# Performance work log

Measured on AMD Instinct MI355X. Metric: run time of the kernel, lower is better.

## Reference

```python
import jax, jax.numpy as jnp
import numpy as np

B, N, D = 8, 2048, 768


def setup_inputs() -> dict:
    key = jax.random.key(0)
    ks = jax.random.split(key, 12)
    s = 1.0 / np.sqrt(D)
    inp = {
        "query": jax.random.normal(ks[0], (B, N, D), dtype=jnp.float32),
        "value": jax.random.normal(ks[1], (B, N, D), dtype=jnp.float32),
        "mask": jax.random.randint(ks[2], (B, N), 0, 2, dtype=jnp.int32),
        "q_w": jax.random.uniform(ks[3], (D, D), jnp.float32, -s, s),
        "q_b": jax.random.uniform(ks[4], (D,), jnp.float32, -s, s),
        "k_w": jax.random.uniform(ks[5], (D, D), jnp.float32, -s, s),
        "k_b": jax.random.uniform(ks[6], (D,), jnp.float32, -s, s),
        "v_w": jax.random.uniform(ks[7], (D, D), jnp.float32, -s, s),
        "v_b": jax.random.uniform(ks[8], (D,), jnp.float32, -s, s),
        "fc_w": jax.random.uniform(ks[9], (D, D), jnp.float32, -s, s),
        "fc_b": jax.random.uniform(ks[10], (D,), jnp.float32, -s, s),
    }
    # guarantee at least one unmasked key per batch to avoid all--inf softmax rows
    inp["mask"] = inp["mask"].at[:, 0].set(1)
    return inp


def reference(query, value, mask, q_w, q_b, k_w, k_b, v_w, v_b, fc_w, fc_b):
    # torch Linear: y = x @ W.T + b  (dim==768 branch of the module)
    q = jnp.einsum("bnd,ed->bne", query, q_w) + q_b   # [B,N,D]
    k = jnp.einsum("bnd,ed->bne", value, k_w) + k_b   # [B,N,D]
    v = jnp.einsum("bnd,ed->bne", value, v_w) + v_b   # [B,N,D]
    # unscaled scores, as in the original (no 1/sqrt(d))
    scores = jnp.einsum("bqd,bkd->bqk", q, k)         # [B,N,N]
    key_mask = mask[:, None, :] != 0                  # [B,1,N]
    scores = jnp.where(key_mask, scores, -jnp.inf)
    attn = jax.nn.softmax(scores, axis=2)
    merged = jnp.einsum("bqk,bkd->bqd", attn, v)      # [B,N,D]
    merged = merged * mask[:, :, None].astype(merged.dtype)
    return jnp.einsum("bnd,ed->bne", merged, fc_w) + fc_b
```

## Files before the change

### kernel.cpp

```cpp
#include <hip/hip_runtime.h>
#include <hip/hip_bf16.h>

using bf16 = __hip_bfloat16;
typedef __attribute__((ext_vector_type(4))) float f32x4;
typedef __attribute__((ext_vector_type(8))) __bf16 bf16x8;
typedef __attribute__((ext_vector_type(4))) unsigned int u32x4;
typedef unsigned short u16;

#define LOG2E 1.4426950408889634f
#define SHIFT2 69.24936192747498f

__device__ __forceinline__ void gload_lds16(const void* g, void* l) {
  __builtin_amdgcn_global_load_lds((const __attribute__((address_space(1))) void*)g,
                                   (__attribute__((address_space(3))) void*)l, 16, 0, 0);
}

__device__ __forceinline__ bf16x8 lds_frag(const bf16* p) {
  u32x4 u = *(const u32x4*)p;
  return __builtin_bit_cast(bf16x8, u);
}

__device__ __forceinline__ u16 bf_bits(float v) {
  return __builtin_bit_cast(u16, __float2bfloat16(v));
}

template<int AMODE, bool SPLIT, int CMODE, bool BIAS, bool RSCALE,
         bool MGATHER, bool CSCAT, bool RAGK, bool NCHECK>
__global__ __launch_bounds__(256, 2) void gemm_nt(
    const void* __restrict__ Ah_, const void* __restrict__ Al_, long lda, long strideA,
    const bf16* __restrict__ Bh_, const bf16* __restrict__ Bl_, long ldb, long strideB,
    void* __restrict__ Ch_, void* __restrict__ Cl_, long ldc, long strideC,
    int Kparam,
    const float* __restrict__ bias,
    float* __restrict__ rowsum, long rsStride,
    const int* __restrict__ idxp, const int* __restrict__ cntp)
{
  const int tid = threadIdx.x;
  const int lane15 = tid & 15;
  const int quad = (tid >> 4) & 3;
  const int wave = tid >> 6;
  const int wm = (wave >> 1) * 64;
  const int wn = (wave & 1) * 64;
  const long z = blockIdx.z;
  const long m0 = (long)blockIdx.y * 128;
  const long n0 = (long)blockIdx.x * 128;

  int cnt = 1 << 30;
  if (cntp) {
    cnt = cntp[z];
    if (m0 >= cnt) return;
    if constexpr (NCHECK) { if (n0 >= cnt) return; }
  }
  const int K = RAGK ? ((cnt + 127) & ~127) : Kparam;

  constexpr int KW = SPLIT ? 64 : 32;
  __shared__ alignas(16) bf16 As[128 * KW];
  __shared__ alignas(16) bf16 Bs[128 * KW];
  __shared__ float rowacc[128];

  const bf16* Bbh = Bh_ + z * strideB;
  const bf16* Bbl = SPLIT ? (Bl_ + z * strideB) : nullptr;

  const bf16* Abh = nullptr; const bf16* Abl = nullptr;
  const float* Af = nullptr;
  if constexpr (AMODE == 0) {
    Abh = (const bf16*)Ah_ + z * strideA;
    if constexpr (SPLIT) Abl = (const bf16*)Al_ + z * strideA;
  } else {
    Af = (const float*)Ah_ + z * strideA;
  }

  const int arow = tid >> 1;
  const int ahalf = tid & 1;
  const int aflip = arow & 1;
  const int aswz = (arow >> 1) & 3;
  long agrow = m0 + arow;
  if constexpr (AMODE == 1 && MGATHER) agrow = idxp[z * 2048 + m0 + arow];

  f32x4 acc[4][4];
  #pragma unroll
  for (int i = 0; i < 4; ++i)
    #pragma unroll
    for (int j = 0; j < 4; ++j) acc[i][j] = (f32x4){0.f, 0.f, 0.f, 0.f};

  for (int k0 = 0; k0 < K; k0 += 32) {
    __syncthreads();
    if constexpr (SPLIT) {
      #pragma unroll
      for (int r = 0; r < 4; ++r) {
        const int idx = r * 256 + tid, row = idx >> 3, slot = idx & 7;
        const int flip = row & 1, sw = (row >> 1) & 3;
        const int h = (slot >> 2) ^ flip, s = (slot & 3) ^ sw;
        const bf16* g = (h ? Bbl : Bbh) + (n0 + row) * ldb + k0 + s * 8;
        gload_lds16(g, &Bs[idx * 8]);
      }
    } else {
      #pragma unroll
      for (int r = 0; r < 2; ++r) {
        const int idx = r * 256 + tid, row = idx >> 2, slot = idx & 3;
        const int sw = (row >> 1) & 3;
        gload_lds16(Bbh + (n0 + row) * ldb + k0 + (slot ^ sw) * 8, &Bs[idx * 8]);
      }
    }
    if constexpr (AMODE == 0) {
      if constexpr (SPLIT) {
        #pragma unroll
        for (int r = 0; r < 4; ++r) {
          const int idx = r * 256 + tid, row = idx >> 3, slot = idx & 7;
          const int flip = row & 1, sw = (row >> 1) & 3;
          const int h = (slot >> 2) ^ flip, s = (slot & 3) ^ sw;
          const bf16* g = (h ? Abl : Abh) + (m0 + row) * lda + k0 + s * 8;
          gload_lds16(g, &As[idx * 8]);
        }
      } else {
        #pragma unroll
        for (int r = 0; r < 2; ++r) {
          const int idx = r * 256 + tid, row = idx >> 2, slot = idx & 3;
          const int sw = (row >> 1) & 3;
          gload_lds16(Abh + (m0 + row) * lda + k0 + (slot ^ sw) * 8, &As[idx * 8]);
        }
      }
    } else {
      const float* src = Af + agrow * lda + k0;
      #pragma unroll
      for (int ss = 0; ss < 2; ++ss) {
        const int s = ahalf * 2 + ss;
        float tv[8];
        *(f32x4*)tv       = *(const f32x4*)(src + s * 8);
        *(f32x4*)(tv + 4) = *(const f32x4*)(src + s * 8 + 4);
        u32x4 hi, lo;
        u16* ph = (u16*)&hi; u16* pl = (u16*)&lo;
        #pragma unroll
        for (int j = 0; j < 8; ++j) {
          bf16 hb = __float2bfloat16(tv[j]);
          ph[j] = __builtin_bit_cast(u16, hb);
          if constexpr (SPLIT) pl[j] = bf_bits(tv[j] - __bfloat162float(hb));
        }
        if constexpr (SPLIT) {
          const int sh = (aflip << 2) | (s ^ aswz);
          *(u32x4*)&As[arow * 64 + sh * 8] = hi;
          *(u32x4*)&As[arow * 64 + (sh ^ 4) * 8] = lo;
        } else {
          *(u32x4*)&As[arow * 32 + (s ^ aswz) * 8] = hi;
        }
      }
    }
    __syncthreads();

    const int swl = (lane15 >> 1) & 3;
    if constexpr (SPLIT) {
      const int eff = ((lane15 & 1) << 2) | (quad ^ swl);
      bf16x8 ah[4], al[4], bh[4], bl[4];
      #pragma unroll
      for (int t = 0; t < 4; ++t) {
        const int ar = (wm + t * 16 + lane15) * 64;
        const int br = (wn + t * 16 + lane15) * 64;
        ah[t] = lds_frag(&As[ar + eff * 8]);
        al[t] = lds_frag(&As[ar + (eff ^ 4) * 8]);
        bh[t] = lds_frag(&Bs[br + eff * 8]);
        bl[t] = lds_frag(&Bs[br + (eff ^ 4) * 8]);
      }
      #pragma unroll
      for (int i = 0; i < 4; ++i)
        #pragma unroll
        for (int j = 0; j < 4; ++j) {
          acc[i][j] = __builtin_amdgcn_mfma_f32_16x16x32_bf16(ah[i], bh[j], acc[i][j], 0, 0, 0);
          acc[i][j] = __builtin_amdgcn_mfma_f32_16x16x32_bf16(al[i], bh[j], acc[i][j], 0, 0, 0);
          acc[i][j] = __builtin_amdgcn_mfma_f32_16x16x32_bf16(ah[i], bl[j], acc[i][j], 0, 0, 0);
        }
    } else {
      const int eff = quad ^ swl;
      bf16x8 ah[4], bh[4];
      #pragma unroll
      for (int t = 0; t < 4; ++t) ah[t] = lds_frag(&As[(wm + t * 16 + lane15) * 32 + eff * 8]);
      #pragma unroll
      for (int t = 0; t < 4; ++t) bh[t] = lds_frag(&Bs[(wn + t * 16 + lane15) * 32 + eff * 8]);
      #pragma unroll
      for (int i = 0; i < 4; ++i)
        #pragma unroll
        for (int j = 0; j < 4; ++j)
          acc[i][j] = __builtin_amdgcn_mfma_f32_16x16x32_bf16(ah[i], bh[j], acc[i][j], 0, 0, 0);
    }
  }

  const long crow0 = m0 + wm + quad * 4;
  const long ccol0 = n0 + wn + lane15;

  if constexpr (CMODE == 3) {
    bf16* P = (bf16*)Ch_ + z * strideC;
    if (tid < 128) rowacc[tid] = 0.f;
    __syncthreads();
    bool keep[4];
    #pragma unroll
    for (int tn = 0; tn < 4; ++tn) keep[tn] = (ccol0 + tn * 16) < cnt;
    #pragma unroll
    for (int tm = 0; tm < 4; ++tm) {
      #pragma unroll
      for (int r = 0; r < 4; ++r) {
        const long row = crow0 + tm * 16 + r;
        float rsum = 0.f;
        #pragma unroll
        for (int tn = 0; tn < 4; ++tn) {
          float p = keep[tn] ? exp2f(fmaf(acc[tm][tn][r], LOG2E, -SHIFT2)) : 0.f;
          bf16 pb = __float2bfloat16(p);
          P[row * ldc + ccol0 + tn * 16] = pb;
          rsum += __bfloat162float(pb);
        }
        atomicAdd(&rowacc[(int)(row - m0)], rsum);
      }
    }
    __syncthreads();
    if (tid < 128) atomicAdd(&rowsum[z * rsStride + m0 + tid], rowacc[tid]);
    return;
  }

  float bv[4] = {0.f, 0.f, 0.f, 0.f};
  if constexpr (BIAS) {
    #pragma unroll
    for (int tn = 0; tn < 4; ++tn) bv[tn] = bias[ccol0 + tn * 16];
  }
  if constexpr (CMODE == 2) {
    float* C = (float*)Ch_ + z * strideC;
    #pragma unroll
    for (int tm = 0; tm < 4; ++tm) {
      #pragma unroll
      for (int r = 0; r < 4; ++r) {
        const long row = crow0 + tm * 16 + r;
        long orow = row;
        bool doStore = true;
        if constexpr (CSCAT) {
          doStore = row < cnt;
          orow = doStore ? (long)idxp[z * 2048 + row] : 0;
        }
        if (doStore) {
          #pragma unroll
          for (int tn = 0; tn < 4; ++tn)
            C[orow * ldc + ccol0 + tn * 16] = acc[tm][tn][r] + bv[tn];
        }
      }
    }
  } else if constexpr (CMODE == 1) {
    bf16* Ch = (bf16*)Ch_ + z * strideC;
    bf16* Cl = (bf16*)Cl_ + z * strideC;
    #pragma unroll
    for (int tm = 0; tm < 4; ++tm) {
      const long row = crow0 + tm * 16;
      #pragma unroll
      for (int tn = 0; tn < 4; ++tn) {
        const long col = ccol0 + tn * 16;
        #pragma unroll
        for (int r = 0; r < 4; ++r) {
          float val = acc[tm][tn][r] + bv[tn];
          bf16 h = __float2bfloat16(val);
          Ch[(row + r) * ldc + col] = h;
          Cl[(row + r) * ldc + col] = __float2bfloat16(val - __bfloat162float(h));
        }
      }
    }
  } else {
    bf16* Ch = (bf16*)Ch_ + z * strideC;
    #pragma unroll
    for (int tm = 0; tm < 4; ++tm) {
      const long row = crow0 + tm * 16;
      float rm[4];
      #pragma unroll
      for (int r = 0; r < 4; ++r) {
        float f = 1.f;
        if constexpr (RSCALE) f = 1.0f / rowsum[z * rsStride + row + r];
        rm[r] = f;
      }
      #pragma unroll
      for (int tn = 0; tn < 4; ++tn) {
        const long col = ccol0 + tn * 16;
        #pragma unroll
        for (int r = 0; r < 4; ++r)
          Ch[(row + r) * ldc + col] = __float2bfloat16((acc[tm][tn][r] + bv[tn]) * rm[r]);
      }
    }
  }
}

__global__ __launch_bounds__(256) void compact_kernel(
    const int* __restrict__ mask, int* __restrict__ idx, int* __restrict__ cnt)
{
  const int z = blockIdx.x, tid = threadIdx.x;
  const int* m = mask + (long)z * 2048;
  int* id = idx + (long)z * 2048;
  int v[8]; int c = 0;
  #pragma unroll
  for (int j = 0; j < 8; ++j) { v[j] = m[tid * 8 + j]; c += (v[j] != 0) ? 1 : 0; }
  __shared__ int sc[256];
  sc[tid] = c;
  __syncthreads();
  for (int off = 1; off < 256; off <<= 1) {
    int y = 0;
    if (tid >= off) y = sc[tid - off];
    __syncthreads();
    if (tid >= off) sc[tid] += y;
    __syncthreads();
  }
  int k = sc[tid] - c;
  #pragma unroll
  for (int j = 0; j < 8; ++j)
    if (v[j]) id[k++] = tid * 8 + j;
  __syncthreads();
  const int tot = sc[255];
  if (tid == 0) cnt[z] = tot;
  const int last = id[tot - 1];
  for (int i = tot + tid; i < 2048; i += 256) id[i] = last;
}

__global__ __launch_bounds__(256) void cvt4_kernel(
    const float* __restrict__ qw, const float* __restrict__ kw,
    const float* __restrict__ vw, const float* __restrict__ fw,
    bf16* __restrict__ Wqh, bf16* __restrict__ Wql,
    bf16* __restrict__ Wkh, bf16* __restrict__ Wkl,
    bf16* __restrict__ Wvh, bf16* __restrict__ Wfh, int n8)
{
  const int i = blockIdx.x * 256 + threadIdx.x;
  if (i >= n8) return;
  const float* in; bf16* oh; bf16* ol = nullptr;
  switch (blockIdx.y) {
    case 0:  in = qw; oh = Wqh; ol = Wql; break;
    case 1:  in = kw; oh = Wkh; ol = Wkl; break;
    case 2:  in = vw; oh = Wvh; break;
    default: in = fw; oh = Wfh; break;
  }
  float tv[8];
  *(f32x4*)tv       = ((const f32x4*)in)[2 * i];
  *(f32x4*)(tv + 4) = ((const f32x4*)in)[2 * i + 1];
  u32x4 H, L;
  u16* ph = (u16*)&H; u16* pl = (u16*)&L;
  #pragma unroll
  for (int j = 0; j < 8; ++j) {
    bf16 hb = __float2bfloat16(tv[j]);
    ph[j] = __builtin_bit_cast(u16, hb);
    pl[j] = bf_bits(tv[j] - __bfloat162float(hb));
  }
  ((u32x4*)oh)[i] = H;
  if (ol) ((u32x4*)ol)[i] = L;
}

__global__ __launch_bounds__(256) void bias_fill_kernel(
    float* __restrict__ out, const float* __restrict__ fc_b)
{
  const long i = (long)blockIdx.x * 256 + threadIdx.x;
  const int col4 = (int)(i % 192);
  ((f32x4*)out)[i] = *(const f32x4*)(fc_b + col4 * 4);
}

__global__ __launch_bounds__(256) void transpose_kernel(
    const u16* __restrict__ in, u16* __restrict__ out, const int* __restrict__ cnt)
{
  const long z = blockIdx.z;
  const long r0 = (long)blockIdx.x * 64, c0 = (long)blockIdx.y * 64;
  const int kb = (cnt[z] + 127) & ~127;
  if (r0 >= kb) return;
  __shared__ alignas(16) u16 t[64][72];
  const u16* inz = in + z * 2048 * 768;
  u16* outz = out + z * 768 * 2048;
  const int tid = threadIdx.x;
  const int rr = tid >> 3, cs = (tid & 7) * 8;
  #pragma unroll
  for (int i = 0; i < 2; ++i) {
    const int row = rr + i * 32;
    u32x4 v = *(const u32x4*)(inz + (r0 + row) * 768 + c0 + cs);
    *(u32x4*)&t[row][cs] = v;
  }
  __syncthreads();
  #pragma unroll
  for (int i = 0; i < 2; ++i) {
    const int oc = rr + i * 32;
    u32x4 o;
    u16* po = (u16*)&o;
    #pragma unroll
    for (int j = 0; j < 8; ++j) po[j] = t[cs + j][oc];
    *(u32x4*)(outz + (c0 + oc) * 2048 + r0 + cs) = o;
  }
}

extern "C" void kernel_launch(void* const* d_in, const int* in_sizes, int n_in,
                              void* d_out, int out_size, void* d_ws, size_t ws_size,
                              hipStream_t stream) {
  const float* query = (const float*)d_in[0];
  const float* value = (const float*)d_in[1];
  const int*   mask  = (const int*)d_in[2];
  const float* q_w   = (const float*)d_in[3];
  const float* q_b   = (const float*)d_in[4];
  const float* k_w   = (const float*)d_in[5];
  const float* k_b   = (const float*)d_in[6];
  const float* v_w   = (const float*)d_in[7];
  const float* v_b   = (const float*)d_in[8];
  const float* fc_w  = (const float*)d_in[9];
  const float* fc_b  = (const float*)d_in[10];

  const long N = 2048, D = 768;
  const long BD = N * D;
  const int WN = (int)(D * D), W8 = WN / 8;

  char* wp = (char*)d_ws;
  auto take = [&](size_t bytes) {
    char* p = wp;
    wp += (bytes + 255) & ~(size_t)255;
    return p;
  };
  bf16* Wqh = (bf16*)take((size_t)WN * 2);
  bf16* Wql = (bf16*)take((size_t)WN * 2);
  bf16* Wkh = (bf16*)take((size_t)WN * 2);
  bf16* Wkl = (bf16*)take((size_t)WN * 2);
  bf16* Wvh = (bf16*)take((size_t)WN * 2);
  bf16* Wfh = (bf16*)take((size_t)WN * 2);
  bf16* Qh = (bf16*)take((size_t)8 * BD * 2);
  bf16* Ql = (bf16*)take((size_t)8 * BD * 2);
  bf16* Kh = (bf16*)take((size_t)8 * BD * 2);
  bf16* Kl = (bf16*)take((size_t)8 * BD * 2);
  bf16* VT = (bf16*)take((size_t)8 * BD * 2);
  bf16* P  = (bf16*)take((size_t)8 * N * N * 2);
  float* rowsum = (float*)take((size_t)8 * N * sizeof(float));
  int* idx = (int*)take((size_t)8 * N * sizeof(int));
  int* cnt = (int*)take(64);
  bf16* V = (bf16*)((char*)P + (size_t)8 * N * N * 2 - (size_t)8 * BD * 2);
  bf16* merged = Qh;

  dim3 blk(256);

  compact_kernel<<<dim3(8), blk, 0, stream>>>(mask, idx, cnt);
  cvt4_kernel<<<dim3(288, 4), blk, 0, stream>>>(q_w, k_w, v_w, fc_w,
      Wqh, Wql, Wkh, Wkl, Wvh, Wfh, W8);
  hipMemsetAsync(rowsum, 0, (size_t)8 * N * sizeof(float), stream);
  bias_fill_kernel<<<dim3(12288), blk, 0, stream>>>((float*)d_out, fc_b);

  gemm_nt<1, true, 1, true, false, true, false, false, false><<<dim3(6, 16, 8), blk, 0, stream>>>(
      query, nullptr, D, BD, Wqh, Wql, D, 0, Qh, Ql, D, BD, (int)D,
      q_b, nullptr, 0, idx, cnt);
  gemm_nt<1, true, 1, true, false, true, false, false, false><<<dim3(6, 16, 8), blk, 0, stream>>>(
      value, nullptr, D, BD, Wkh, Wkl, D, 0, Kh, Kl, D, BD, (int)D,
      k_b, nullptr, 0, idx, cnt);
  gemm_nt<1, false, 0, true, false, true, false, false, false><<<dim3(6, 16, 8), blk, 0, stream>>>(
      value, nullptr, D, BD, Wvh, nullptr, D, 0, V, nullptr, D, BD, (int)D,
      v_b, nullptr, 0, idx, cnt);
  transpose_kernel<<<dim3(32, 12, 8), blk, 0, stream>>>((const u16*)V, (u16*)VT, cnt);

  gemm_nt<0, true, 3, false, false, false, false, false, true><<<dim3(16, 16, 8), blk, 0, stream>>>(
      Qh, Ql, D, BD, Kh, Kl, D, BD, P, nullptr, N, N * N, (int)D,
      nullptr, rowsum, N, nullptr, cnt);
  gemm_nt<0, false, 0, false, true, false, false, true, false><<<dim3(6, 16, 8), blk, 0, stream>>>(
      P, nullptr, N, N * N, VT, nullptr, N, BD, merged, nullptr, D, BD, 0,
      nullptr, rowsum, N, nullptr, cnt);
  gemm_nt<0, false, 2, true, false, false, true, false, false><<<dim3(6, 16, 8), blk, 0, stream>>>(
      merged, nullptr, D, BD, Wfh, nullptr, D, 0, d_out, nullptr, D, BD, (int)D,
      fc_b, nullptr, 0, idx, cnt);
}
```

Measured before the change: 456.1 us.

## Use persistent compacted tile scheduling for GEMMs and fuse Q/K projections

Converts the batched GEMM kernel into a persistent-grid kernel that enumerates only the valid tiles per batch, derived from the masked-row counts, and loops over them with a fixed 512-block grid. Early-exit blocks for padded rows and columns are no longer launched. The Q and K projection GEMMs are merged into one launch through secondary pointers. The per-tile linear search over batch prefix sums and the extra syncs add some overhead, and fixed grid sizing may leave load imbalance.

```diff
diff --git a/kernel.cpp b/kernel.cpp
--- a/kernel.cpp
+++ b/kernel.cpp
@@ -24,16 +24,21 @@
   return __builtin_bit_cast(u16, __float2bfloat16(v));
 }
 
+struct GArgs {
+  const void* Ah; const void* Al; long lda; long strideA;
+  const bf16* Bh; const bf16* Bl; long ldb; long strideB;
+  void* Ch; void* Cl; long ldc; long strideC;
+  int K;
+  const float* bias;
+  float* rowsum; long rsStride;
+  const int* idx; const int* cnt;
+  const void* Ah2; const bf16* Bh2; const bf16* Bl2;
+  void* Ch2; void* Cl2; const float* bias2;
+};
+
 template<int AMODE, bool SPLIT, int CMODE, bool BIAS, bool RSCALE,
-         bool MGATHER, bool CSCAT, bool RAGK, bool NCHECK>
-__global__ __launch_bounds__(256, 2) void gemm_nt(
-    const void* __restrict__ Ah_, const void* __restrict__ Al_, long lda, long strideA,
-    const bf16* __restrict__ Bh_, const bf16* __restrict__ Bl_, long ldb, long strideB,
-    void* __restrict__ Ch_, void* __restrict__ Cl_, long ldc, long strideC,
-    int Kparam,
-    const float* __restrict__ bias,
-    float* __restrict__ rowsum, long rsStride,
-    const int* __restrict__ idxp, const int* __restrict__ cntp)
+         bool MGATHER, bool CSCAT, bool SQUARE, bool RAGK, bool QK2>
+__global__ __launch_bounds__(256, 2) void gemm_nt(GArgs ga)
 {
   const int tid = threadIdx.x;
   const int lane15 = tid & 15;
@@ -41,240 +46,265 @@
   const int wave = tid >> 6;
   const int wm = (wave >> 1) * 64;
   const int wn = (wave & 1) * 64;
-  const long z = blockIdx.z;
-  const long m0 = (long)blockIdx.y * 128;
-  const long n0 = (long)blockIdx.x * 128;
-
-  int cnt = 1 << 30;
-  if (cntp) {
-    cnt = cntp[z];
-    if (m0 >= cnt) return;
-    if constexpr (NCHECK) { if (n0 >= cnt) return; }
-  }
-  const int K = RAGK ? ((cnt + 127) & ~127) : Kparam;
-
+
+  constexpr int NZ = QK2 ? 16 : 8;
   constexpr int KW = SPLIT ? 64 : 32;
   __shared__ alignas(16) bf16 As[128 * KW];
   __shared__ alignas(16) bf16 Bs[128 * KW];
   __shared__ float rowacc[128];
-
-  const bf16* Bbh = Bh_ + z * strideB;
-  const bf16* Bbl = SPLIT ? (Bl_ + z * strideB) : nullptr;
-
-  const bf16* Abh = nullptr; const bf16* Abl = nullptr;
-  const float* Af = nullptr;
-  if constexpr (AMODE == 0) {
-    Abh = (const bf16*)Ah_ + z * strideA;
-    if constexpr (SPLIT) Abl = (const bf16*)Al_ + z * strideA;
-  } else {
-    Af = (const float*)Ah_ + z * strideA;
-  }
+  __shared__ int sT[8];
+  __shared__ int sTz[NZ];
+
+  if (tid < 8) sT[tid] = (ga.cnt[tid] + 127) >> 7;
+  __syncthreads();
+  if (tid < NZ) {
+    const int Tm = sT[QK2 ? (tid & 7) : tid];
+    sTz[tid] = SQUARE ? Tm * Tm : Tm * 6;
+  }
+  __syncthreads();
+  int total = 0;
+  #pragma unroll
+  for (int i = 0; i < NZ; ++i) total += sTz[i];
 
   const int arow = tid >> 1;
   const int ahalf = tid & 1;
   const int aflip = arow & 1;
   const int aswz = (arow >> 1) & 3;
-  long agrow = m0 + arow;
-  if constexpr (AMODE == 1 && MGATHER) agrow = idxp[z * 2048 + m0 + arow];
-
-  f32x4 acc[4][4];
-  #pragma unroll
-  for (int i = 0; i < 4; ++i)
+
+  for (int t = blockIdx.x; t < total; t += gridDim.x) {
+    int vz = 0, rem = t;
+    while (rem >= sTz[vz]) { rem -= sTz[vz]; ++vz; }
+    const int z = QK2 ? (vz & 7) : vz;
+    const int mat = QK2 ? (vz >> 3) : 0;
+    const int Tm = sT[z];
+    int mt, nt;
+    if constexpr (SQUARE) { mt = rem / Tm; nt = rem - mt * Tm; }
+    else                  { mt = rem / 6;  nt = rem - mt * 6; }
+    const long m0 = (long)mt * 128;
+    const long n0 = (long)nt * 128;
+    const int cnt = ga.cnt[z];
+    const int K = RAGK ? Tm * 128 : ga.K;
+
+    const bf16* Bh = (QK2 && mat) ? ga.Bh2 : ga.Bh;
+    const bf16* Bl = (QK2 && mat) ? ga.Bl2 : ga.Bl;
+    const bf16* Bbh = Bh + z * ga.strideB;
+    const bf16* Bbl = SPLIT ? (Bl + z * ga.strideB) : nullptr;
+
+    const bf16* Abh = nullptr; const bf16* Abl = nullptr;
+    const float* Af = nullptr;
+    {
+      const void* Ahp = (QK2 && mat) ? ga.Ah2 : ga.Ah;
+      if constexpr (AMODE == 0) {
+        Abh = (const bf16*)Ahp + (long)z * ga.strideA;
+        if constexpr (SPLIT) Abl = (const bf16*)ga.Al + (long)z * ga.strideA;
+      } else {
+        Af = (const float*)Ahp + (long)z * ga.strideA;
+      }
+    }
+    long agrow = m0 + arow;
+    if constexpr (AMODE == 1 && MGATHER) agrow = ga.idx[(long)z * 2048 + m0 + arow];
+
+    f32x4 acc[4][4];
     #pragma unroll
-    for (int j = 0; j < 4; ++j) acc[i][j] = (f32x4){0.f, 0.f, 0.f, 0.f};
-
-  for (int k0 = 0; k0 < K; k0 += 32) {
-    __syncthreads();
-    if constexpr (SPLIT) {
-      #pragma unroll
-      for (int r = 0; r < 4; ++r) {
-        const int idx = r * 256 + tid, row = idx >> 3, slot = idx & 7;
-        const int flip = row & 1, sw = (row >> 1) & 3;
-        const int h = (slot >> 2) ^ flip, s = (slot & 3) ^ sw;
-        const bf16* g = (h ? Bbl : Bbh) + (n0 + row) * ldb + k0 + s * 8;
-        gload_lds16(g, &Bs[idx * 8]);
-      }
-    } else {
-      #pragma unroll
-      for (int r = 0; r < 2; ++r) {
-        const int idx = r * 256 + tid, row = idx >> 2, slot = idx & 3;
-        const int sw = (row >> 1) & 3;
-        gload_lds16(Bbh + (n0 + row) * ldb + k0 + (slot ^ sw) * 8, &Bs[idx * 8]);
-      }
-    }
-    if constexpr (AMODE == 0) {
+    for (int i = 0; i < 4; ++i)
+      #pragma unroll
+      for (int j = 0; j < 4; ++j) acc[i][j] = (f32x4){0.f, 0.f, 0.f, 0.f};
+
+    for (int k0 = 0; k0 < K; k0 += 32) {
+      __syncthreads();
       if constexpr (SPLIT) {
         #pragma unroll
         for (int r = 0; r < 4; ++r) {
           const int idx = r * 256 + tid, row = idx >> 3, slot = idx & 7;
           const int flip = row & 1, sw = (row >> 1) & 3;
           const int h = (slot >> 2) ^ flip, s = (slot & 3) ^ sw;
-          const bf16* g = (h ? Abl : Abh) + (m0 + row) * lda + k0 + s * 8;
-          gload_lds16(g, &As[idx * 8]);
+          const bf16* g = (h ? Bbl : Bbh) + (n0 + row) * ga.ldb + k0 + s * 8;
+          gload_lds16(g, &Bs[idx * 8]);
         }
       } else {
         #pragma unroll
         for (int r = 0; r < 2; ++r) {
           const int idx = r * 256 + tid, row = idx >> 2, slot = idx & 3;
           const int sw = (row >> 1) & 3;
-          gload_lds16(Abh + (m0 + row) * lda + k0 + (slot ^ sw) * 8, &As[idx * 8]);
+          gload_lds16(Bbh + (n0 + row) * ga.ldb + k0 + (slot ^ sw) * 8, &Bs[idx * 8]);
+        }
+      }
+      if constexpr (AMODE == 0) {
+        if constexpr (SPLIT) {
+          #pragma unroll
+          for (int r = 0; r < 4; ++r) {
+            const int idx = r * 256 + tid, row = idx >> 3, slot = idx & 7;
+            const int flip = row & 1, sw = (row >> 1) & 3;
+            const int h = (slot >> 2) ^ flip, s = (slot & 3) ^ sw;
+            const bf16* g = (h ? Abl : Abh) + (m0 + row) * ga.lda + k0 + s * 8;
+            gload_lds16(g, &As[idx * 8]);
+          }
+        } else {
+          #pragma unroll
+          for (int r = 0; r < 2; ++r) {
+            const int idx = r * 256 + tid, row = idx >> 2, slot = idx & 3;
+            const int sw = (row >> 1) & 3;
+            gload_lds16(Abh + (m0 + row) * ga.lda + k0 + (slot ^ sw) * 8, &As[idx * 8]);
+          }
+        }
+      } else {
+        const float* src = Af + agrow * ga.lda + k0;
+        #pragma unroll
+        for (int ss = 0; ss < 2; ++ss) {
+          const int s = ahalf * 2 + ss;
+          float tv[8];
+          *(f32x4*)tv       = *(const f32x4*)(src + s * 8);
+          *(f32x4*)(tv + 4) = *(const f32x4*)(src + s * 8 + 4);
+          u32x4 hi, lo;
+          u16* ph = (u16*)&hi; u16* pl = (u16*)&lo;
+          #pragma unroll
+          for (int j = 0; j < 8; ++j) {
+            bf16 hb = __float2bfloat16(tv[j]);
+            ph[j] = __builtin_bit_cast(u16, hb);
+            if constexpr (SPLIT) pl[j] = bf_bits(tv[j] - __bfloat162float(hb));
+          }
+          if constexpr (SPLIT) {
+            const int sh = (aflip << 2) | (s ^ aswz);
+            *(u32x4*)&As[arow * 64 + sh * 8] = hi;
+            *(u32x4*)&As[arow * 64 + (sh ^ 4) * 8] = lo;
+          } else {
+            *(u32x4*)&As[arow * 32 + (s ^ aswz) * 8] = hi;
+          }
+        }
+      }
+      __syncthreads();
+
+      const int swl = (lane15 >> 1) & 3;
+      if constexpr (SPLIT) {
+        const int eff = ((lane15 & 1) << 2) | (quad ^ swl);
+        bf16x8 ah[4], al[4], bh[4], bl[4];
+        #pragma unroll
+        for (int tt = 0; tt < 4; ++tt) {
+          const int ar = (wm + tt * 16 + lane15) * 64;
+          const int br = (wn + tt * 16 + lane15) * 64;
+          ah[tt] = lds_frag(&As[ar + eff * 8]);
+          al[tt] = lds_frag(&As[ar + (eff ^ 4) * 8]);
+          bh[tt] = lds_frag(&Bs[br + eff * 8]);
+          bl[tt] = lds_frag(&Bs[br + (eff ^ 4) * 8]);
+        }
+        #pragma unroll
+        for (int i = 0; i < 4; ++i)
+          #pragma unroll
+          for (int j = 0; j < 4; ++j) {
+            acc[i][j] = __builtin_amdgcn_mfma_f32_16x16x32_bf16(ah[i], bh[j], acc[i][j], 0, 0, 0);
+            acc[i][j] = __builtin_amdgcn_mfma_f32_16x16x32_bf16(al[i], bh[j], acc[i][j], 0, 0, 0);
+            acc[i][j] = __builtin_amdgcn_mfma_f32_16x16x32_bf16(ah[i], bl[j], acc[i][j], 0, 0, 0);
+          }
+      } else {
+        const int eff = quad ^ swl;
+        bf16x8 ah[4], bh[4];
+        #pragma unroll
+        for (int tt = 0; tt < 4; ++tt) ah[tt] = lds_frag(&As[(wm + tt * 16 + lane15) * 32 + eff * 8]);
+        #pragma unroll
+        for (int tt = 0; tt < 4; ++tt) bh[tt] = lds_frag(&Bs[(wn + tt * 16 + lane15) * 32 + eff * 8]);
+        #pragma unroll
+        for (int i = 0; i < 4; ++i)
+          #pragma unroll
+          for (int j = 0; j < 4; ++j)
+            acc[i][j] = __builtin_amdgcn_mfma_f32_16x16x32_bf16(ah[i], bh[j], acc[i][j], 0, 0, 0);
+      }
+    }
+
+    const long crow0 = m0 + wm + quad * 4;
+    const long ccol0 = n0 + wn + lane15;
+
+    if constexpr (CMODE == 3) {
+      bf16* P = (bf16*)ga.Ch + (long)z * ga.strideC;
+      __syncthreads();
+      if (tid < 128) rowacc[tid] = 0.f;
+      __syncthreads();
+      bool keep[4];
+      #pragma unroll
+      for (int tn = 0; tn < 4; ++tn) keep[tn] = (ccol0 + tn * 16) < cnt;
+      #pragma unroll
+      for (int tm = 0; tm < 4; ++tm) {
+        #pragma unroll
+        for (int r = 0; r < 4; ++r) {
+          const long row = crow0 + tm * 16 + r;
+          float rsum = 0.f;
+          #pragma unroll
+          for (int tn = 0; tn < 4; ++tn) {
+            float p = keep[tn] ? exp2f(fmaf(acc[tm][tn][r], LOG2E, -SHIFT2)) : 0.f;
+            bf16 pb = __float2bfloat16(p);
+            P[row * ga.ldc + ccol0 + tn * 16] = pb;
+            rsum += __bfloat162float(pb);
+          }
+          atomicAdd(&rowacc[(int)(row - m0)], rsum);
+        }
+      }
+      __syncthreads();
+      if (tid < 128) atomicAdd(&ga.rowsum[z * ga.rsStride + m0 + tid], rowacc[tid]);
+      continue;
+    }
+
+    const float* bias = (QK2 && mat) ? ga.bias2 : ga.bias;
+    float bv[4] = {0.f, 0.f, 0.f, 0.f};
+    if constexpr (BIAS) {
+      #pragma unroll
+      for (int tn = 0; tn < 4; ++tn) bv[tn] = bias[ccol0 + tn * 16];
+    }
+    if constexpr (CMODE == 2) {
+      float* C = (float*)ga.Ch + (long)z * ga.strideC;
+      #pragma unroll
+      for (int tm = 0; tm < 4; ++tm) {
+        #pragma unroll
+        for (int r = 0; r < 4; ++r) {
+          const long row = crow0 + tm * 16 + r;
+          long orow = row;
+          bool doStore = true;
+          if constexpr (CSCAT) {
+            doStore = row < cnt;
+            orow = doStore ? (long)ga.idx[(long)z * 2048 + row] : 0;
+          }
+          if (doStore) {
+            #pragma unroll
+            for (int tn = 0; tn < 4; ++tn)
+              C[orow * ga.ldc + ccol0 + tn * 16] = acc[tm][tn][r] + bv[tn];
+          }
+        }
+      }
+    } else if constexpr (CMODE == 1) {
+      bf16* Ch = (bf16*)((QK2 && mat) ? ga.Ch2 : ga.Ch) + (long)z * ga.strideC;
+      bf16* Cl = (bf16*)((QK2 && mat) ? ga.Cl2 : ga.Cl) + (long)z * ga.strideC;
+      #pragma unroll
+      for (int tm = 0; tm < 4; ++tm) {
+        const long row = crow0 + tm * 16;
+        #pragma unroll
+        for (int tn = 0; tn < 4; ++tn) {
+          const long col = ccol0 + tn * 16;
+          #pragma unroll
+          for (int r = 0; r < 4; ++r) {
+            float val = acc[tm][tn][r] + bv[tn];
+            bf16 h = __float2bfloat16(val);
+            Ch[(row + r) * ga.ldc + col] = h;
+            Cl[(row + r) * ga.ldc + col] = __float2bfloat16(val - __bfloat162float(h));
+          }
         }
       }
     } else {
-      const float* src = Af + agrow * lda + k0;
-      #pragma unroll
-      for (int ss = 0; ss < 2; ++ss) {
-        const int s = ahalf * 2 + ss;
-        float tv[8];
-        *(f32x4*)tv       = *(const f32x4*)(src + s * 8);
-        *(f32x4*)(tv + 4) = *(const f32x4*)(src + s * 8 + 4);
-        u32x4 hi, lo;
-        u16* ph = (u16*)&hi; u16* pl = (u16*)&lo;
-        #pragma unroll
-        for (int j = 0; j < 8; ++j) {
-          bf16 hb = __float2bfloat16(tv[j]);
-          ph[j] = __builtin_bit_cast(u16, hb);
-          if constexpr (SPLIT) pl[j] = bf_bits(tv[j] - __bfloat162float(hb));
-        }
-        if constexpr (SPLIT) {
-          const int sh = (aflip << 2) | (s ^ aswz);
-          *(u32x4*)&As[arow * 64 + sh * 8] = hi;
-          *(u32x4*)&As[arow * 64 + (sh ^ 4) * 8] = lo;
-        } else {
-          *(u32x4*)&As[arow * 32 + (s ^ aswz) * 8] = hi;
-        }
-      }
-    }
-    __syncthreads();
-
-    const int swl = (lane15 >> 1) & 3;
-    if constexpr (SPLIT) {
-      const int eff = ((lane15 & 1) << 2) | (quad ^ swl);
-      bf16x8 ah[4], al[4], bh[4], bl[4];
-      #pragma unroll
-      for (int t = 0; t < 4; ++t) {
-        const int ar = (wm + t * 16 + lane15) * 64;
-        const int br = (wn + t * 16 + lane15) * 64;
-        ah[t] = lds_frag(&As[ar + eff * 8]);
-        al[t] = lds_frag(&As[ar + (eff ^ 4) * 8]);
-        bh[t] = lds_frag(&Bs[br + eff * 8]);
-        bl[t] = lds_frag(&Bs[br + (eff ^ 4) * 8]);
-      }
-      #pragma unroll
-      for (int i = 0; i < 4; ++i)
-        #pragma unroll
-        for (int j = 0; j < 4; ++j) {
-          acc[i][j] = __builtin_amdgcn_mfma_f32_16x16x32_bf16(ah[i], bh[j], acc[i][j], 0, 0, 0);
-          acc[i][j] = __builtin_amdgcn_mfma_f32_16x16x32_bf16(al[i], bh[j], acc[i][j], 0, 0, 0);
-          acc[i][j] = __builtin_amdgcn_mfma_f32_16x16x32_bf16(ah[i], bl[j], acc[i][j], 0, 0, 0);
-        }
-    } else {
-      const int eff = quad ^ swl;
-      bf16x8 ah[4], bh[4];
-      #pragma unroll
-      for (int t = 0; t < 4; ++t) ah[t] = lds_frag(&As[(wm + t * 16 + lane15) * 32 + eff * 8]);
-      #pragma unroll
-      for (int t = 0; t < 4; ++t) bh[t] = lds_frag(&Bs[(wn + t * 16 + lane15) * 32 + eff * 8]);
-      #pragma unroll
-      for (int i = 0; i < 4; ++i)
-        #pragma unroll
-        for (int j = 0; j < 4; ++j)
-          acc[i][j] = __builtin_amdgcn_mfma_f32_16x16x32_bf16(ah[i], bh[j], acc[i][j], 0, 0, 0);
-    }
-  }
-
-  const long crow0 = m0 + wm + quad * 4;
-  const long ccol0 = n0 + wn + lane15;
-
-  if constexpr (CMODE == 3) {
-    bf16* P = (bf16*)Ch_ + z * strideC;
-    if (tid < 128) rowacc[tid] = 0.f;
-    __syncthreads();
-    bool keep[4];
-    #pragma unroll
-    for (int tn = 0; tn < 4; ++tn) keep[tn] = (ccol0 + tn * 16) < cnt;
-    #pragma unroll
-    for (int tm = 0; tm < 4; ++tm) {
-      #pragma unroll
-      for (int r = 0; r < 4; ++r) {
-        const long row = crow0 + tm * 16 + r;
-        float rsum = 0.f;
+      bf16* Ch = (bf16*)ga.Ch + (long)z * ga.strideC;
+      #pragma unroll
+      for (int tm = 0; tm < 4; ++tm) {
+        const long row = crow0 + tm * 16;
+        float rm[4];
+        #pragma unroll
+        for (int r = 0; r < 4; ++r) {
+          float f = 1.f;
+          if constexpr (RSCALE) f = 1.0f / ga.rowsum[z * ga.rsStride + row + r];
+          rm[r] = f;
+        }
         #pragma unroll
         for (int tn = 0; tn < 4; ++tn) {
-          float p = keep[tn] ? exp2f(fmaf(acc[tm][tn][r], LOG2E, -SHIFT2)) : 0.f;
-          bf16 pb = __float2bfloat16(p);
-          P[row * ldc + ccol0 + tn * 16] = pb;
-          rsum += __bfloat162float(pb);
-        }
-        atomicAdd(&rowacc[(int)(row - m0)], rsum);
-      }
-    }
-    __syncthreads();
-    if (tid < 128) atomicAdd(&rowsum[z * rsStride + m0 + tid], rowacc[tid]);
-    return;
-  }
-
-  float bv[4] = {0.f, 0.f, 0.f, 0.f};
-  if constexpr (BIAS) {
-    #pragma unroll
-    for (int tn = 0; tn < 4; ++tn) bv[tn] = bias[ccol0 + tn * 16];
-  }
-  if constexpr (CMODE == 2) {
-    float* C = (float*)Ch_ + z * strideC;
-    #pragma unroll
-    for (int tm = 0; tm < 4; ++tm) {
-      #pragma unroll
-      for (int r = 0; r < 4; ++r) {
-        const long row = crow0 + tm * 16 + r;
-        long orow = row;
-        bool doStore = true;
-        if constexpr (CSCAT) {
-          doStore = row < cnt;
-          orow = doStore ? (long)idxp[z * 2048 + row] : 0;
-        }
-        if (doStore) {
-          #pragma unroll
-          for (int tn = 0; tn < 4; ++tn)
-            C[orow * ldc + ccol0 + tn * 16] = acc[tm][tn][r] + bv[tn];
-        }
-      }
-    }
-  } else if constexpr (CMODE == 1) {
-    bf16* Ch = (bf16*)Ch_ + z * strideC;
-    bf16* Cl = (bf16*)Cl_ + z * strideC;
-    #pragma unroll
-    for (int tm = 0; tm < 4; ++tm) {
-      const long row = crow0 + tm * 16;
-      #pragma unroll
-      for (int tn = 0; tn < 4; ++tn) {
-        const long col = ccol0 + tn * 16;
-        #pragma unroll
-        for (int r = 0; r < 4; ++r) {
-          float val = acc[tm][tn][r] + bv[tn];
-          bf16 h = __float2bfloat16(val);
-          Ch[(row + r) * ldc + col] = h;
-          Cl[(row + r) * ldc + col] = __float2bfloat16(val - __bfloat162float(h));
-        }
-      }
-    }
-  } else {
-    bf16* Ch = (bf16*)Ch_ + z * strideC;
-    #pragma unroll
-    for (int tm = 0; tm < 4; ++tm) {
-      const long row = crow0 + tm * 16;
-      float rm[4];
-      #pragma unroll
-      for (int r = 0; r < 4; ++r) {
-        float f = 1.f;
-        if constexpr (RSCALE) f = 1.0f / rowsum[z * rsStride + row + r];
-        rm[r] = f;
-      }
-      #pragma unroll
-      for (int tn = 0; tn < 4; ++tn) {
-        const long col = ccol0 + tn * 16;
-        #pragma unroll
-        for (int r = 0; r < 4; ++r)
-          Ch[(row + r) * ldc + col] = __float2bfloat16((acc[tm][tn][r] + bv[tn]) * rm[r]);
+          const long col = ccol0 + tn * 16;
+          #pragma unroll
+          for (int r = 0; r < 4; ++r)
+            Ch[(row + r) * ga.ldc + col] = __float2bfloat16((acc[tm][tn][r] + bv[tn]) * rm[r]);
+        }
       }
     }
   }
@@ -423,6 +453,7 @@
   bf16* merged = Qh;
 
   dim3 blk(256);
+  dim3 g512(512);
 
   compact_kernel<<<dim3(8), blk, 0, stream>>>(mask, idx, cnt);
   cvt4_kernel<<<dim3(288, 4), blk, 0, stream>>>(q_w, k_w, v_w, fc_w,
@@ -430,24 +461,40 @@
   hipMemsetAsync(rowsum, 0, (size_t)8 * N * sizeof(float), stream);
   bias_fill_kernel<<<dim3(12288), blk, 0, stream>>>((float*)d_out, fc_b);
 
-  gemm_nt<1, true, 1, true, false, true, false, false, false><<<dim3(6, 16, 8), blk, 0, stream>>>(
-      query, nullptr, D, BD, Wqh, Wql, D, 0, Qh, Ql, D, BD, (int)D,
-      q_b, nullptr, 0, idx, cnt);
-  gemm_nt<1, true, 1, true, false, true, false, false, false><<<dim3(6, 16, 8), blk, 0, stream>>>(
-      value, nullptr, D, BD, Wkh, Wkl, D, 0, Kh, Kl, D, BD, (int)D,
-      k_b, nullptr, 0, idx, cnt);
-  gemm_nt<1, false, 0, true, false, true, false, false, false><<<dim3(6, 16, 8), blk, 0, stream>>>(
-      value, nullptr, D, BD, Wvh, nullptr, D, 0, V, nullptr, D, BD, (int)D,
-      v_b, nullptr, 0, idx, cnt);
+  GArgs a{};
+  a.idx = idx; a.cnt = cnt; a.rowsum = rowsum; a.rsStride = N;
+
+  a.Ah = query; a.Al = nullptr; a.lda = D; a.strideA = BD;
+  a.Bh = Wqh; a.Bl = Wql; a.ldb = D; a.strideB = 0;
+  a.Ch = Qh; a.Cl = Ql; a.ldc = D; a.strideC = BD;
+  a.K = (int)D; a.bias = q_b;
+  a.Ah2 = value; a.Bh2 = Wkh; a.Bl2 = Wkl; a.Ch2 = Kh; a.Cl2 = Kl; a.bias2 = k_b;
+  gemm_nt<1, true, 1, true, false, true, false, false, false, true>
+      <<<g512, blk, 0, stream>>>(a);
+
+  a.Ah = value; a.Bh = Wvh; a.Bl = nullptr;
+  a.Ch = V; a.Cl = nullptr; a.bias = v_b;
+  gemm_nt<1, false, 0, true, false, true, false, false, false, false>
+      <<<g512, blk, 0, stream>>>(a);
   transpose_kernel<<<dim3(32, 12, 8), blk, 0, stream>>>((const u16*)V, (u16*)VT, cnt);
 
-  gemm_nt<0, true, 3, false, false, false, false, false, true><<<dim3(16, 16, 8), blk, 0, stream>>>(
-      Qh, Ql, D, BD, Kh, Kl, D, BD, P, nullptr, N, N * N, (int)D,
-      nullptr, rowsum, N, nullptr, cnt);
-  gemm_nt<0, false, 0, false, true, false, false, true, false><<<dim3(6, 16, 8), blk, 0, stream>>>(
-      P, nullptr, N, N * N, VT, nullptr, N, BD, merged, nullptr, D, BD, 0,
-      nullptr, rowsum, N, nullptr, cnt);
-  gemm_nt<0, false, 2, true, false, false, true, false, false><<<dim3(6, 16, 8), blk, 0, stream>>>(
-      merged, nullptr, D, BD, Wfh, nullptr, D, 0, d_out, nullptr, D, BD, (int)D,
-      fc_b, nullptr, 0, idx, cnt);
-}
+  a.Ah = Qh; a.Al = Ql; a.lda = D; a.strideA = BD;
+  a.Bh = Kh; a.Bl = Kl; a.ldb = D; a.strideB = BD;
+  a.Ch = P; a.Cl = nullptr; a.ldc = N; a.strideC = N * N;
+  a.K = (int)D; a.bias = nullptr;
+  gemm_nt<0, true, 3, false, false, false, false, true, false, false>
+      <<<g512, blk, 0, stream>>>(a);
+
+  a.Ah = P; a.Al = nullptr; a.lda = N; a.strideA = N * N;
+  a.Bh = VT; a.Bl = nullptr; a.ldb = N; a.strideB = BD;
+  a.Ch = merged; a.Cl = nullptr; a.ldc = D; a.strideC = BD;
+  gemm_nt<0, false, 0, false, true, false, false, false, true, false>
+      <<<g512, blk, 0, stream>>>(a);
+
+  a.Ah = merged; a.lda = D; a.strideA = BD;
+  a.Bh = Wfh; a.Bl = nullptr; a.ldb = D; a.strideB = 0;
+  a.Ch = d_out; a.Cl = nullptr; a.ldc = D; a.strideC = BD;
+  a.K = (int)D; a.bias = fc_b;
+  gemm_nt<0, false, 2, true, false, false, true, false, false, false>
+      <<<g512, blk, 0, stream>>>(a);
+}
```

Result: faster. 439.4 us (-3.7%).
